# Kernel tuning notes

Hardware: AMD Instinct MI355X
Metric: run time of the kernel (lower is better)

The kernel has to match this reference:

```python
import jax, jax.numpy as jnp
import numpy as np
import math

B, N, C = 4, 4096, 1024
H, K_LM = 16, 256
HEAD_DIM = C // H


def setup_inputs() -> dict:
    key = jax.random.key(0)
    k1, k2, k3, k4, k5 = jax.random.split(key, 5)
    x = jax.random.normal(k1, (B, N, C), dtype=jnp.float32)
    Wqkv = jax.random.normal(k2, (3 * C, C), dtype=jnp.float32) * 0.02
    E = jax.random.normal(k3, (H, K_LM, N), dtype=jnp.float32) * 0.02
    Wproj = jax.random.normal(k4, (C, C), dtype=jnp.float32) * 0.02
    bproj = jax.random.normal(k5, (C,), dtype=jnp.float32) * 0.02
    return {"x": x, "Wqkv": Wqkv, "E": E, "Wproj": Wproj, "bproj": bproj}


def reference(x, Wqkv, E, Wproj, bproj):
    Bsz, n, c = x.shape
    h, d = H, c // H
    # qkv projection (no bias): [B,N,3C] -> (3,B,H,N,d)
    qkv = (x @ Wqkv.T).reshape(Bsz, n, 3, h, d).transpose(2, 0, 3, 1, 4)
    q, k, v = qkv[0], qkv[1], qkv[2]
    # Linformer landmark projection: E[h,k,n] @ K/V[b,h,n,d] -> [b,h,k,d]
    k_lm = jnp.einsum('hkn,bhnd->bhkd', E, k)
    v_lm = jnp.einsum('hkn,bhnd->bhkd', E, v)
    # scaled dot + softmax over landmarks: [b,h,n,k]
    dot = jnp.einsum('bhnd,bhkd->bhnk', q, k_lm) / math.sqrt(d)
    attn = jax.nn.softmax(dot, axis=-1)
    # weighted sum; faithful to original: reshape (B,H,N,d) -> (B,N,C) WITHOUT head transpose
    out = jnp.einsum('bhnk,bhkd->bhnd', attn, v_lm).reshape(Bsz, n, c)
    # output projection (dropouts are identity at eval / p=0)
    return out @ Wproj.T + bproj
```

## Files before the change

### kernel.cpp

```cpp
#include <hip/hip_runtime.h>


typedef unsigned short ushort_t;
typedef float f32x4 __attribute__((ext_vector_type(4)));
typedef __bf16 bf16x8 __attribute__((ext_vector_type(8)));
typedef unsigned short ushort8 __attribute__((ext_vector_type(8)));
typedef unsigned short ushort4_t __attribute__((ext_vector_type(4)));

__device__ inline ushort_t f2bf(float f) {
  unsigned int u = __float_as_uint(f);
  u += 0x7fff + ((u >> 16) & 1);
  return (ushort_t)(u >> 16);
}

__device__ inline void gload_lds16(const ushort_t* g, ushort_t* l) {
  __builtin_amdgcn_global_load_lds(
      (const __attribute__((address_space(1))) void*)g,
      (__attribute__((address_space(3))) void*)l, 16, 0, 0);
}

__global__ __launch_bounds__(256) void cvt_all(
    const float* __restrict__ x,  ushort_t* __restrict__ xo,
    const float* __restrict__ w1, ushort_t* __restrict__ w1o,
    const float* __restrict__ e,  ushort_t* __restrict__ eo,
    const float* __restrict__ w2, ushort_t* __restrict__ w2o) {
  int i = blockIdx.x * blockDim.x + threadIdx.x;
  const float* in; ushort_t* out; int idx;
  if (i < 4194304)               { in = x;  out = xo;  idx = i; }
  else if (i < 4980736)          { in = w1; out = w1o; idx = i - 4194304; }
  else if (i < 9175040)          { in = e;  out = eo;  idx = i - 4980736; }
  else                           { in = w2; out = w2o; idx = i - 9175040; }
  float4 v = ((const float4*)in)[idx];
  ushort4_t o;
  o.x = f2bf(v.x); o.y = f2bf(v.y); o.z = f2bf(v.z); o.w = f2bf(v.w);
  ((ushort4_t*)out)[idx] = o;
}


#define BARX __builtin_amdgcn_s_barrier()
#define WVM(n) do { asm volatile("s_waitcnt vmcnt(" #n ")" ::: "memory"); \
                    __builtin_amdgcn_sched_barrier(0); } while (0)
#define WLG  do { asm volatile("s_waitcnt lgkmcnt(0)" ::: "memory"); \
                  __builtin_amdgcn_sched_barrier(0); } while (0)

#define STG_A(h, slot, tt) do { \
    gload_lds16(sA[h][0] + (tt) * 64, (ushort_t*)(smem + (slot) * 32768 + (h) * 16384 + (w * 2 + 0) * 1024)); \
    gload_lds16(sA[h][1] + (tt) * 64, (ushort_t*)(smem + (slot) * 32768 + (h) * 16384 + (w * 2 + 1) * 1024)); \
  } while (0)
#define STG_B(h, slot, tt) do { \
    gload_lds16(sB[h][0] + (tt) * 64, (ushort_t*)(smem + 65536 + (slot) * 32768 + (h) * 16384 + (w * 2 + 0) * 1024)); \
    gload_lds16(sB[h][1] + (tt) * 64, (ushort_t*)(smem + 65536 + (slot) * 32768 + (h) * 16384 + (w * 2 + 1) * 1024)); \
  } while (0)

#define RD_A(mh) do { \
    const char* ba_ = smem + sl * 32768 + ((mh) * 128 + wm * 64 + l15) * 128; \
    _Pragma("unroll") for (int i_ = 0; i_ < 4; i_++) { \
      aF[i_][0] = *(const bf16x8*)(ba_ + i_ * 2048 + cs0); \
      aF[i_][1] = *(const bf16x8*)(ba_ + i_ * 2048 + cs1); } \
  } while (0)
#define RD_B(nh) do { \
    const char* bb_ = smem + 65536 + sl * 32768 + ((nh) * 128 + wn * 32 + l15) * 128; \
    _Pragma("unroll") for (int j_ = 0; j_ < 2; j_++) { \
      bF[j_][0] = *(const bf16x8*)(bb_ + j_ * 2048 + cs0); \
      bF[j_][1] = *(const bf16x8*)(bb_ + j_ * 2048 + cs1); } \
  } while (0)

#define MQ(mh, nh) do { \
    _Pragma("unroll") for (int i_ = 0; i_ < 4; i_++) \
    _Pragma("unroll") for (int j_ = 0; j_ < 2; j_++) { \
      acc[(mh) * 4 + i_][(nh) * 2 + j_] = __builtin_amdgcn_mfma_f32_16x16x32_bf16( \
          aF[i_][0], bF[j_][0], acc[(mh) * 4 + i_][(nh) * 2 + j_], 0, 0, 0); \
      acc[(mh) * 4 + i_][(nh) * 2 + j_] = __builtin_amdgcn_mfma_f32_16x16x32_bf16( \
          aF[i_][1], bF[j_][1], acc[(mh) * 4 + i_][(nh) * 2 + j_], 0, 0, 0); } \
  } while (0)

__device__ __attribute__((always_inline)) inline void pipe256(
    const ushort_t* __restrict__ Ag, const ushort_t* __restrict__ Bg,
    long long m0, long long n0, char* smem, f32x4 acc[8][4]) {
  const int tid = threadIdx.x, lane = tid & 63, w = tid >> 6;
  const int l15 = lane & 15, quad = lane >> 4;
  const int wm = w >> 2, wn = w & 3;
  const int sw = l15 & 7;
  const int K = 1024;
  const int cs0 = ((0 * 4 + quad) ^ sw) << 4;
  const int cs1 = ((1 * 4 + quad) ^ sw) << 4;
  const int lr8 = lane >> 3;
  const int sdat = ((lane & 7) ^ lr8) * 8;
  const ushort_t* sA[2][2];
  const ushort_t* sB[2][2];
#pragma unroll
  for (int h = 0; h < 2; h++)
#pragma unroll
    for (int q = 0; q < 2; q++) {
      sA[h][q] = Ag + (m0 + h * 128 + (w * 2 + q) * 8 + lr8) * K + sdat;
      sB[h][q] = Bg + (n0 + h * 128 + (w * 2 + q) * 8 + lr8) * K + sdat;
    }

  const f32x4 zz = {0.f, 0.f, 0.f, 0.f};
#pragma unroll
  for (int i = 0; i < 8; i++)
#pragma unroll
    for (int j = 0; j < 4; j++) acc[i][j] = zz;

  bf16x8 aF[4][2];
  bf16x8 bF[2][2];

  STG_A(0, 0, 0); STG_B(0, 0, 0); STG_A(1, 0, 0); STG_B(1, 0, 0);
  WVM(4);
  BARX;

#pragma unroll 2
  for (int t = 0; t < 16; ++t) {
    const int sl = t & 1, sn = sl ^ 1;
    const bool pf = (t < 15);
    RD_A(0); RD_B(0);
    if (pf) STG_A(0, sn, t + 1);
    BARX; WLG;
    __builtin_amdgcn_s_setprio(1); MQ(0, 0); __builtin_amdgcn_s_setprio(0);
    if (pf) { WVM(4); } else { WVM(2); }
    BARX;
    RD_A(1);
    if (pf) STG_B(0, sn, t + 1);
    BARX; WLG;
    __builtin_amdgcn_s_setprio(1); MQ(1, 0); __builtin_amdgcn_s_setprio(0);
    if (pf) { WVM(4); } else { WVM(0); }
    BARX;
    RD_B(1);
    if (pf) STG_A(1, sn, t + 1);
    BARX; WLG;
    __builtin_amdgcn_s_setprio(1); MQ(1, 1); __builtin_amdgcn_s_setprio(0);
    BARX;
    RD_A(0);
    if (pf) STG_B(1, sn, t + 1);
    BARX; WLG;
    __builtin_amdgcn_s_setprio(1); MQ(0, 1); __builtin_amdgcn_s_setprio(0);
    if (pf) WVM(4);
    BARX;
  }
}

__global__ __launch_bounds__(512) void gemm_qkv(
    const ushort_t* __restrict__ A, const ushort_t* __restrict__ W,
    ushort_t* __restrict__ q, ushort_t* __restrict__ kT, ushort_t* __restrict__ vT) {
  __shared__ __align__(16) char smem[131072];
  const int lin = blockIdx.x;
  const int xcd = lin & 7, rr_ = lin >> 3;
  const int mt = xcd * 8 + (rr_ & 7);
  const int nt = rr_ >> 3;
  const long long m0 = (long long)mt * 256;
  const long long n0 = (long long)nt * 256;

  f32x4 acc[8][4];
  pipe256(A, W, m0, n0, smem, acc);

  const int tid = threadIdx.x, lane = tid & 63, w = tid >> 6;
  const int l15 = lane & 15, quad = lane >> 4;
  const int wm = w >> 2, wn = w & 3;
  const int b     = (int)(m0 >> 12);
  const int nrow0 = (int)(m0 & 4095);
  const int s     = (int)(n0 >> 10);
  const int ncol0 = (int)(n0 & 1023);
  const int h0    = ncol0 >> 6;

  if (s == 0) {
#pragma unroll
    for (int mh = 0; mh < 2; mh++)
#pragma unroll
      for (int i = 0; i < 4; i++)
#pragma unroll
        for (int nh = 0; nh < 2; nh++)
#pragma unroll
          for (int j = 0; j < 2; j++) {
            int cx = ncol0 + nh * 128 + wn * 32 + j * 16;
            int h  = cx >> 6;
            int dd = (cx & 63) + l15;
            long long z = (long long)b * 16 + h;
            int nb = nrow0 + mh * 128 + wm * 64 + i * 16 + quad * 4;
#pragma unroll
            for (int r = 0; r < 4; r++)
              q[z * 262144 + (long long)(nb + r) * 64 + dd] = f2bf(acc[mh * 4 + i][nh * 2 + j][r]);
          }
  } else {
    ushort_t (*T)[136] = (ushort_t(*)[136])smem;
    ushort_t* KV = (s == 1) ? kT : vT;
#pragma unroll
    for (int p = 0; p < 2; p++) {
      __syncthreads();
#pragma unroll
      for (int i = 0; i < 4; i++)
#pragma unroll
        for (int nh = 0; nh < 2; nh++)
#pragma unroll
          for (int j = 0; j < 2; j++) {
            int c = nh * 128 + wn * 32 + j * 16 + l15;
            int t = wm * 64 + i * 16 + quad * 4;
            ushort4_t o = {f2bf(acc[p * 4 + i][nh * 2 + j][0]), f2bf(acc[p * 4 + i][nh * 2 + j][1]),
                           f2bf(acc[p * 4 + i][nh * 2 + j][2]), f2bf(acc[p * 4 + i][nh * 2 + j][3])};
            *(ushort4_t*)(&T[c][t]) = o;
          }
      __syncthreads();
#pragma unroll
      for (int it = 0; it < 8; it++) {
        int ch = it * 512 + tid;
        int cl = ch >> 4, tc = (ch & 15) * 8;
        ushort8 v = *(const ushort8*)(&T[cl][tc]);
        int h = h0 + (cl >> 6), dd = cl & 63;
        long long z = (long long)b * 16 + h;
        *(ushort8*)(KV + z * 262144 + (long long)dd * 4096 + (nrow0 + p * 128 + tc)) = v;
      }
    }
  }
}

__global__ __launch_bounds__(256) void lm_gemm(
    const ushort_t* __restrict__ E, const ushort_t* __restrict__ kT,
    const ushort_t* __restrict__ vT, float* __restrict__ pK, float* __restrict__ pV) {
  __shared__ __align__(16) ushort_t smem[12288];
  const int tid = threadIdx.x, lane = tid & 63, w = tid >> 6;
  const int l15 = lane & 15, quad = lane >> 4;
  const int kt = blockIdx.x;
  const int s  = blockIdx.y;
  const int z  = blockIdx.z;
  const int h  = z & 15;
  const int lr = lane >> 2, lc = (lane & 3) * 8;

  const ushort_t* gE = E  + ((long long)h * 256 + kt * 64 + 16 * w + lr) * 4096 + s * 1024 + lc;
  const ushort_t* gK = kT + ((long long)z * 64 + 16 * w + lr) * 4096 + s * 1024 + lc;
  const ushort_t* gV = vT + ((long long)z * 64 + 16 * w + lr) * 4096 + s * 1024 + lc;
  ushort_t* lE = smem + 512 * w;
  ushort_t* lK = smem + 4096 + 512 * w;
  ushort_t* lV = smem + 8192 + 512 * w;

  const f32x4 zz = {0.f, 0.f, 0.f, 0.f};
  f32x4 aK[4], aV[4];
#pragma unroll
  for (int j = 0; j < 4; j++) { aK[j] = zz; aV[j] = zz; }

  for (int n = 0; n < 1024; n += 64) {
    __syncthreads();
#pragma unroll
    for (int p = 0; p < 2; p++) {
      gload_lds16(gE + n + 32 * p, lE + p * 2048);
      gload_lds16(gK + n + 32 * p, lK + p * 2048);
      gload_lds16(gV + n + 32 * p, lV + p * 2048);
    }
    __syncthreads();
#pragma unroll
    for (int p = 0; p < 2; p++) {
      bf16x8 ef = *(const bf16x8*)(smem + p * 2048 + (w * 16 + l15) * 32 + quad * 8);
#pragma unroll
      for (int j = 0; j < 4; j++) {
        bf16x8 kf = *(const bf16x8*)(smem + 4096 + p * 2048 + (j * 16 + l15) * 32 + quad * 8);
        aK[j] = __builtin_amdgcn_mfma_f32_16x16x32_bf16(ef, kf, aK[j], 0, 0, 0);
        bf16x8 vf = *(const bf16x8*)(smem + 8192 + p * 2048 + (j * 16 + l15) * 32 + quad * 8);
        aV[j] = __builtin_amdgcn_mfma_f32_16x16x32_bf16(ef, vf, aV[j], 0, 0, 0);
      }
    }
  }

  float* oK = pK + ((long long)(z * 4 + s) * 256 + kt * 64) * 64;
  float* oV = pV + ((long long)(z * 4 + s) * 256 + kt * 64) * 64;
#pragma unroll
  for (int j = 0; j < 4; j++)
#pragma unroll
    for (int r = 0; r < 4; r++) {
      int row = w * 16 + quad * 4 + r, col = j * 16 + l15;
      oK[row * 64 + col] = aK[j][r];
      oV[row * 64 + col] = aV[j][r];
    }
}

__global__ __launch_bounds__(256) void lm_reduce(
    const float* __restrict__ pK, const float* __restrict__ pV,
    ushort_t* __restrict__ klm, ushort_t* __restrict__ vlmT) {
  __shared__ float Tv[64][68];
  const int tid = threadIdx.x;
  const int kt = blockIdx.x;
  const int z  = blockIdx.y;
  const long long base = (long long)z * 4 * 16384 + kt * 64 * 64;
  const int row = tid >> 2, c0 = (tid & 3) * 16;

  float sk[16];
#pragma unroll
  for (int g = 0; g < 4; g++) {
    f32x4 a = {0.f, 0.f, 0.f, 0.f};
#pragma unroll
    for (int s = 0; s < 4; s++)
      a += *(const f32x4*)(pK + base + (long long)s * 16384 + row * 64 + c0 + g * 4);
    sk[g * 4 + 0] = a[0]; sk[g * 4 + 1] = a[1]; sk[g * 4 + 2] = a[2]; sk[g * 4 + 3] = a[3];
  }
  {
    ushort_t* dst = klm + ((long long)z * 256 + kt * 64 + row) * 64 + c0;
    ushort8 o0, o1;
#pragma unroll
    for (int i = 0; i < 8; i++) { o0[i] = f2bf(sk[i]); o1[i] = f2bf(sk[8 + i]); }
    *(ushort8*)(dst) = o0;
    *(ushort8*)(dst + 8) = o1;
  }

#pragma unroll
  for (int g = 0; g < 4; g++) {
    f32x4 a = {0.f, 0.f, 0.f, 0.f};
#pragma unroll
    for (int s = 0; s < 4; s++)
      a += *(const f32x4*)(pV + base + (long long)s * 16384 + row * 64 + c0 + g * 4);
    *(f32x4*)(&Tv[row][c0 + g * 4]) = a;
  }
  __syncthreads();
  {
    ushort8 o0, o1;
#pragma unroll
    for (int i = 0; i < 8; i++) {
      o0[i] = f2bf(Tv[c0 + i][row]);
      o1[i] = f2bf(Tv[c0 + 8 + i][row]);
    }
    ushort_t* dst = vlmT + ((long long)z * 64 + row) * 256 + kt * 64 + c0;
    *(ushort8*)(dst) = o0;
    *(ushort8*)(dst + 8) = o1;
  }
}

__global__ __launch_bounds__(256) void attn_fused(
    const ushort_t* __restrict__ Q, const ushort_t* __restrict__ Klm,
    const ushort_t* __restrict__ VlmT, ushort_t* __restrict__ O) {
  __shared__ __align__(16) ushort_t smem[16896];
  ushort_t (*As)[40]  = (ushort_t(*)[40])smem;
  ushort_t (*Bs)[40]  = (ushort_t(*)[40])(smem + 2560);
  ushort_t (*P)[264]  = (ushort_t(*)[264])smem;
  const int tid = threadIdx.x, lane = tid & 63, w = tid >> 6;
  const int l15 = lane & 15, quad = lane >> 4;
  const int z = blockIdx.z;
  const long long m0 = (long long)blockIdx.x * 64;
  const ushort_t* Qb = Q + (long long)z * 262144;
  const ushort_t* Kb = Klm + (long long)z * 16384;
  const ushort_t* Vb = VlmT + (long long)z * 16384;

  const f32x4 zz = {0.f, 0.f, 0.f, 0.f};
  f32x4 acc[16];
#pragma unroll
  for (int j = 0; j < 16; j++) acc[j] = zz;

  const int sr = tid >> 2, sc = (tid & 3) * 8;

  for (int kt = 0; kt < 2; kt++) {
    const int k0 = kt * 32;
    ushort8 av = *(const ushort8*)(Qb + (m0 + sr) * 64 + k0 + sc);
    ushort8 bv[4];
#pragma unroll
    for (int r = 0; r < 4; r++) {
      int c = r * 256 + tid;
      bv[r] = *(const ushort8*)(Kb + (c >> 2) * 64 + k0 + (c & 3) * 8);
    }
    __syncthreads();
    *(ushort8*)(&As[sr][sc]) = av;
#pragma unroll
    for (int r = 0; r < 4; r++) {
      int c = r * 256 + tid;
      *(ushort8*)(&Bs[c >> 2][(c & 3) * 8]) = bv[r];
    }
    __syncthreads();
    bf16x8 af = *(const bf16x8*)(&As[w * 16 + l15][quad * 8]);
#pragma unroll
    for (int j = 0; j < 16; j++) {
      bf16x8 bfj = *(const bf16x8*)(&Bs[j * 16 + l15][quad * 8]);
      acc[j] = __builtin_amdgcn_mfma_f32_16x16x32_bf16(af, bfj, acc[j], 0, 0, 0);
    }
  }

  __syncthreads();
#pragma unroll
  for (int r = 0; r < 4; r++) {
    float x[16];
    float vmax = -1e30f;
#pragma unroll
    for (int j = 0; j < 16; j++) { x[j] = acc[j][r] * 0.125f; vmax = fmaxf(vmax, x[j]); }
#pragma unroll
    for (int m = 1; m < 16; m <<= 1) vmax = fmaxf(vmax, __shfl_xor(vmax, m, 64));
    float s = 0.f;
#pragma unroll
    for (int j = 0; j < 16; j++) { x[j] = __expf(x[j] - vmax); s += x[j]; }
#pragma unroll
    for (int m = 1; m < 16; m <<= 1) s += __shfl_xor(s, m, 64);
    float inv = 1.0f / s;
    int row = w * 16 + quad * 4 + r;
#pragma unroll
    for (int j = 0; j < 16; j++)
      P[row][j * 16 + l15] = f2bf(x[j] * inv);
  }
  __syncthreads();

  f32x4 o_acc[4];
#pragma unroll
  for (int j = 0; j < 4; j++) o_acc[j] = zz;
#pragma unroll
  for (int kc = 0; kc < 8; kc++) {
    bf16x8 pf = *(const bf16x8*)(&P[w * 16 + l15][kc * 32 + quad * 8]);
#pragma unroll
    for (int j = 0; j < 4; j++) {
      bf16x8 vf = *(const bf16x8*)(Vb + (j * 16 + l15) * 256 + kc * 32 + quad * 8);
      o_acc[j] = __builtin_amdgcn_mfma_f32_16x16x32_bf16(pf, vf, o_acc[j], 0, 0, 0);
    }
  }

#pragma unroll
  for (int j = 0; j < 4; j++)
#pragma unroll
    for (int r = 0; r < 4; r++) {
      int row = w * 16 + quad * 4 + r;
      int col = j * 16 + l15;
      O[(long long)z * 262144 + (m0 + row) * 64 + col] = f2bf(o_acc[j][r]);
    }
}

__global__ __launch_bounds__(512) void gemm_nt_256(
    const ushort_t* __restrict__ A, const ushort_t* __restrict__ B,
    float* __restrict__ C, const float* __restrict__ bias) {
  __shared__ __align__(16) char smem[131072];
  const int lin = blockIdx.x;
  const int xcd = lin & 7, rr_ = lin >> 3;
  const int mt = xcd * 8 + (rr_ & 7);
  const int nt = rr_ >> 3;
  const long long m0 = (long long)mt * 256;
  const long long n0 = (long long)nt * 256;

  f32x4 acc[8][4];
  pipe256(A, B, m0, n0, smem, acc);

  const int tid = threadIdx.x, lane = tid & 63, w = tid >> 6;
  const int l15 = lane & 15, quad = lane >> 4;
  const int wm = w >> 2, wn = w & 3;

#pragma unroll
  for (int mh = 0; mh < 2; mh++)
#pragma unroll
    for (int i = 0; i < 4; i++)
#pragma unroll
      for (int nh = 0; nh < 2; nh++)
#pragma unroll
        for (int j = 0; j < 2; j++) {
          long long row = m0 + mh * 128 + wm * 64 + i * 16 + quad * 4;
          long long col = n0 + nh * 128 + wn * 32 + j * 16 + l15;
          float bv = bias[col];
#pragma unroll
          for (int r = 0; r < 4; r++)
            C[(row + r) * 1024 + col] = acc[mh * 4 + i][nh * 2 + j][r] + bv;
        }
}

extern "C" void kernel_launch(void* const* d_in, const int* in_sizes, int n_in,
                              void* d_out, int out_size, void* d_ws, size_t ws_size,
                              hipStream_t stream) {
  const float* x     = (const float*)d_in[0];
  const float* Wqkv  = (const float*)d_in[1];
  const float* E     = (const float*)d_in[2];
  const float* Wproj = (const float*)d_in[3];
  const float* bproj = (const float*)d_in[4];
  float* out = (float*)d_out;

  char* ws = (char*)d_ws;
  ushort_t* x_bf     = (ushort_t*)(ws + 0);
  float*    pK       = (float*)   (ws + 0);
  float*    pV       = (float*)   (ws + 16777216);
  ushort_t* wqkv_bf  = (ushort_t*)(ws + 33554432);
  ushort_t* e_bf     = (ushort_t*)(ws + 39845888);
  ushort_t* wproj_bf = (ushort_t*)(ws + 73400320);
  ushort_t* q_bf     = (ushort_t*)(ws + 75497472);
  ushort_t* kT       = (ushort_t*)(ws + 109051904);
  ushort_t* vT       = (ushort_t*)(ws + 142606336);
  ushort_t* klm      = (ushort_t*)(ws + 176160768);
  ushort_t* vlmT     = (ushort_t*)(ws + 178257920);

  cvt_all<<<36864, 256, 0, stream>>>(x, x_bf, Wqkv, wqkv_bf, E, e_bf, Wproj, wproj_bf);

  gemm_qkv<<<768, 512, 0, stream>>>(x_bf, wqkv_bf, q_bf, kT, vT);

  lm_gemm<<<dim3(4, 4, 64), 256, 0, stream>>>(e_bf, kT, vT, pK, pV);

  lm_reduce<<<dim3(4, 64), 256, 0, stream>>>(pK, pV, klm, vlmT);

  attn_fused<<<dim3(64, 1, 64), 256, 0, stream>>>(q_bf, klm, vlmT, x_bf);

  gemm_nt_256<<<256, 512, 0, stream>>>(x_bf, wproj_bf, out, bproj);
}
```

Measured before the change: 451.8 us.

## Fuse landmark GEMM with reduction and reorder GEMM pipeline sub-tile schedule

Replaces the split-K landmark projection (lm_gemm plus lm_reduce through fp32 partial buffers) with a single lm_fused kernel. Each block now loops over the full N, double-buffers its LDS with async global-to-LDS loads, uses swizzled LDS addressing, and remaps blocks so each XCD handles a contiguous set of heads. This removes the fp32 partial round-trip and one launch, at the cost of fewer blocks (256) each running a longer serial loop. Separately, the main 256x256 GEMM pipeline keeps two B fragments in registers so sub-tiles run in the order (0,0),(0,1),(1,0),(1,1), cutting LDS re-reads. The last iteration is peeled to drop the per-iteration prefetch predicate.

Result: slower. 519.6 us (+15.0%).

```diff
diff --git a/kernel.cpp b/kernel.cpp
--- a/kernel.cpp
+++ b/kernel.cpp
@@ -58,20 +58,20 @@
       aF[i_][0] = *(const bf16x8*)(ba_ + i_ * 2048 + cs0); \
       aF[i_][1] = *(const bf16x8*)(ba_ + i_ * 2048 + cs1); } \
   } while (0)
-#define RD_B(nh) do { \
+#define RD_B(nh, BF) do { \
     const char* bb_ = smem + 65536 + sl * 32768 + ((nh) * 128 + wn * 32 + l15) * 128; \
     _Pragma("unroll") for (int j_ = 0; j_ < 2; j_++) { \
-      bF[j_][0] = *(const bf16x8*)(bb_ + j_ * 2048 + cs0); \
-      bF[j_][1] = *(const bf16x8*)(bb_ + j_ * 2048 + cs1); } \
+      BF[j_][0] = *(const bf16x8*)(bb_ + j_ * 2048 + cs0); \
+      BF[j_][1] = *(const bf16x8*)(bb_ + j_ * 2048 + cs1); } \
   } while (0)
 
-#define MQ(mh, nh) do { \
+#define MQ(mh, nh, BF) do { \
     _Pragma("unroll") for (int i_ = 0; i_ < 4; i_++) \
     _Pragma("unroll") for (int j_ = 0; j_ < 2; j_++) { \
       acc[(mh) * 4 + i_][(nh) * 2 + j_] = __builtin_amdgcn_mfma_f32_16x16x32_bf16( \
-          aF[i_][0], bF[j_][0], acc[(mh) * 4 + i_][(nh) * 2 + j_], 0, 0, 0); \
+          aF[i_][0], BF[j_][0], acc[(mh) * 4 + i_][(nh) * 2 + j_], 0, 0, 0); \
       acc[(mh) * 4 + i_][(nh) * 2 + j_] = __builtin_amdgcn_mfma_f32_16x16x32_bf16( \
-          aF[i_][1], bF[j_][1], acc[(mh) * 4 + i_][(nh) * 2 + j_], 0, 0, 0); } \
+          aF[i_][1], BF[j_][1], acc[(mh) * 4 + i_][(nh) * 2 + j_], 0, 0, 0); } \
   } while (0)
 
 __device__ __attribute__((always_inline)) inline void pipe256(
@@ -103,39 +103,54 @@
     for (int j = 0; j < 4; j++) acc[i][j] = zz;
 
   bf16x8 aF[4][2];
-  bf16x8 bF[2][2];
-
-  STG_A(0, 0, 0); STG_B(0, 0, 0); STG_A(1, 0, 0); STG_B(1, 0, 0);
+  bf16x8 bF0[2][2], bF1[2][2];
+
+  STG_A(0, 0, 0); STG_B(0, 0, 0); STG_B(1, 0, 0); STG_A(1, 0, 0);
   WVM(4);
   BARX;
 
 #pragma unroll 2
-  for (int t = 0; t < 16; ++t) {
+  for (int t = 0; t < 15; ++t) {
     const int sl = t & 1, sn = sl ^ 1;
-    const bool pf = (t < 15);
-    RD_A(0); RD_B(0);
-    if (pf) STG_A(0, sn, t + 1);
-    BARX; WLG;
-    __builtin_amdgcn_s_setprio(1); MQ(0, 0); __builtin_amdgcn_s_setprio(0);
-    if (pf) { WVM(4); } else { WVM(2); }
+    RD_A(0); RD_B(0, bF0);
+    STG_A(0, sn, t + 1);
+    BARX; WLG;
+    __builtin_amdgcn_s_setprio(1); MQ(0, 0, bF0); __builtin_amdgcn_s_setprio(0);
+    WVM(4);
+    BARX;
+    RD_B(1, bF1);
+    STG_B(0, sn, t + 1);
+    BARX; WLG;
+    __builtin_amdgcn_s_setprio(1); MQ(0, 1, bF1); __builtin_amdgcn_s_setprio(0);
+    WVM(4);
     BARX;
     RD_A(1);
-    if (pf) STG_B(0, sn, t + 1);
-    BARX; WLG;
-    __builtin_amdgcn_s_setprio(1); MQ(1, 0); __builtin_amdgcn_s_setprio(0);
-    if (pf) { WVM(4); } else { WVM(0); }
-    BARX;
-    RD_B(1);
-    if (pf) STG_A(1, sn, t + 1);
-    BARX; WLG;
-    __builtin_amdgcn_s_setprio(1); MQ(1, 1); __builtin_amdgcn_s_setprio(0);
-    BARX;
-    RD_A(0);
-    if (pf) STG_B(1, sn, t + 1);
-    BARX; WLG;
-    __builtin_amdgcn_s_setprio(1); MQ(0, 1); __builtin_amdgcn_s_setprio(0);
-    if (pf) WVM(4);
-    BARX;
+    STG_B(1, sn, t + 1);
+    BARX; WLG;
+    __builtin_amdgcn_s_setprio(1); MQ(1, 0, bF0); __builtin_amdgcn_s_setprio(0);
+    BARX;
+    STG_A(1, sn, t + 1);
+    __builtin_amdgcn_s_setprio(1); MQ(1, 1, bF1); __builtin_amdgcn_s_setprio(0);
+    WVM(4);
+    BARX;
+  }
+  {
+    const int sl = 1;
+    RD_A(0); RD_B(0, bF0);
+    BARX; WLG;
+    __builtin_amdgcn_s_setprio(1); MQ(0, 0, bF0); __builtin_amdgcn_s_setprio(0);
+    WVM(2);
+    BARX;
+    RD_B(1, bF1);
+    BARX; WLG;
+    __builtin_amdgcn_s_setprio(1); MQ(0, 1, bF1); __builtin_amdgcn_s_setprio(0);
+    WVM(0);
+    BARX;
+    RD_A(1);
+    BARX; WLG;
+    __builtin_amdgcn_s_setprio(1); MQ(1, 0, bF0); __builtin_amdgcn_s_setprio(0);
+    BARX;
+    __builtin_amdgcn_s_setprio(1); MQ(1, 1, bF1); __builtin_amdgcn_s_setprio(0);
   }
 }
 
@@ -212,102 +227,83 @@
   }
 }
 
-__global__ __launch_bounds__(256) void lm_gemm(
+#define LM_STAGE(s_, n_) do { \
+    ushort_t* b_ = (ushort_t*)(smemc + (s_) * 24576); \
+    _Pragma("unroll") for (int p_ = 0; p_ < 2; p_++) { \
+      gload_lds16(gE + (n_) + 32 * p_, b_ + 512 * w + p_ * 2048); \
+      gload_lds16(gK + (n_) + 32 * p_, b_ + 4096 + 512 * w + p_ * 2048); \
+      gload_lds16(gV + (n_) + 32 * p_, b_ + 8192 + 512 * w + p_ * 2048); \
+    } } while (0)
+
+#define LM_COMP(sl_) do { \
+    const ushort_t* base_ = (const ushort_t*)(smemc + (sl_) * 24576); \
+    _Pragma("unroll") for (int p_ = 0; p_ < 2; p_++) { \
+      bf16x8 ef = *(const bf16x8*)(base_ + p_ * 2048 + (w * 16 + l15) * 32 + ((quad ^ swz) * 8)); \
+      _Pragma("unroll") for (int j_ = 0; j_ < 4; j_++) { \
+        bf16x8 kf = *(const bf16x8*)(base_ + 4096 + p_ * 2048 + (j_ * 16 + l15) * 32 + ((quad ^ swz) * 8)); \
+        aK[j_] = __builtin_amdgcn_mfma_f32_16x16x32_bf16(ef, kf, aK[j_], 0, 0, 0); \
+        bf16x8 vf = *(const bf16x8*)(base_ + 8192 + p_ * 2048 + (j_ * 16 + l15) * 32 + ((quad ^ swz) * 8)); \
+        aV[j_] = __builtin_amdgcn_mfma_f32_16x16x32_bf16(ef, vf, aV[j_], 0, 0, 0); \
+      } } } while (0)
+
+__global__ __launch_bounds__(256) void lm_fused(
     const ushort_t* __restrict__ E, const ushort_t* __restrict__ kT,
-    const ushort_t* __restrict__ vT, float* __restrict__ pK, float* __restrict__ pV) {
-  __shared__ __align__(16) ushort_t smem[12288];
+    const ushort_t* __restrict__ vT, ushort_t* __restrict__ klm,
+    ushort_t* __restrict__ vlmT) {
+  __shared__ __align__(16) char smemc[49152];
   const int tid = threadIdx.x, lane = tid & 63, w = tid >> 6;
   const int l15 = lane & 15, quad = lane >> 4;
-  const int kt = blockIdx.x;
-  const int s  = blockIdx.y;
-  const int z  = blockIdx.z;
+  const int bid = blockIdx.x;
+  const int xcd = bid & 7, loc = bid >> 3;
+  const int z  = xcd * 8 + (loc >> 2);
+  const int kt = loc & 3;
   const int h  = z & 15;
-  const int lr = lane >> 2, lc = (lane & 3) * 8;
-
-  const ushort_t* gE = E  + ((long long)h * 256 + kt * 64 + 16 * w + lr) * 4096 + s * 1024 + lc;
-  const ushort_t* gK = kT + ((long long)z * 64 + 16 * w + lr) * 4096 + s * 1024 + lc;
-  const ushort_t* gV = vT + ((long long)z * 64 + 16 * w + lr) * 4096 + s * 1024 + lc;
-  ushort_t* lE = smem + 512 * w;
-  ushort_t* lK = smem + 4096 + 512 * w;
-  ushort_t* lV = smem + 8192 + 512 * w;
+  const int lr = lane >> 2;
+  const int lc = ((lane & 3) ^ ((lr >> 1) & 3)) * 8;
+  const int swz = (l15 >> 1) & 3;
+
+  const ushort_t* gE = E  + ((long long)h * 256 + kt * 64 + 16 * w + lr) * 4096 + lc;
+  const ushort_t* gK = kT + ((long long)z * 64 + 16 * w + lr) * 4096 + lc;
+  const ushort_t* gV = vT + ((long long)z * 64 + 16 * w + lr) * 4096 + lc;
 
   const f32x4 zz = {0.f, 0.f, 0.f, 0.f};
   f32x4 aK[4], aV[4];
 #pragma unroll
   for (int j = 0; j < 4; j++) { aK[j] = zz; aV[j] = zz; }
 
-  for (int n = 0; n < 1024; n += 64) {
-    __syncthreads();
-#pragma unroll
-    for (int p = 0; p < 2; p++) {
-      gload_lds16(gE + n + 32 * p, lE + p * 2048);
-      gload_lds16(gK + n + 32 * p, lK + p * 2048);
-      gload_lds16(gV + n + 32 * p, lV + p * 2048);
-    }
-    __syncthreads();
-#pragma unroll
-    for (int p = 0; p < 2; p++) {
-      bf16x8 ef = *(const bf16x8*)(smem + p * 2048 + (w * 16 + l15) * 32 + quad * 8);
-#pragma unroll
-      for (int j = 0; j < 4; j++) {
-        bf16x8 kf = *(const bf16x8*)(smem + 4096 + p * 2048 + (j * 16 + l15) * 32 + quad * 8);
-        aK[j] = __builtin_amdgcn_mfma_f32_16x16x32_bf16(ef, kf, aK[j], 0, 0, 0);
-        bf16x8 vf = *(const bf16x8*)(smem + 8192 + p * 2048 + (j * 16 + l15) * 32 + quad * 8);
-        aV[j] = __builtin_amdgcn_mfma_f32_16x16x32_bf16(ef, vf, aV[j], 0, 0, 0);
-      }
-    }
-  }
-
-  float* oK = pK + ((long long)(z * 4 + s) * 256 + kt * 64) * 64;
-  float* oV = pV + ((long long)(z * 4 + s) * 256 + kt * 64) * 64;
+  LM_STAGE(0, 0);
+#pragma unroll 2
+  for (int t = 0; t < 63; ++t) {
+    const int sl = t & 1;
+    LM_STAGE(sl ^ 1, (t + 1) * 64);
+    WVM(6);
+    BARX;
+    LM_COMP(sl);
+    BARX;
+  }
+  WVM(0);
+  BARX;
+  LM_COMP(1);
+
+  ushort_t* oK = klm + ((long long)z * 256 + kt * 64) * 64;
 #pragma unroll
   for (int j = 0; j < 4; j++)
 #pragma unroll
     for (int r = 0; r < 4; r++) {
       int row = w * 16 + quad * 4 + r, col = j * 16 + l15;
-      oK[row * 64 + col] = aK[j][r];
-      oV[row * 64 + col] = aV[j][r];
-    }
-}
-
-__global__ __launch_bounds__(256) void lm_reduce(
-    const float* __restrict__ pK, const float* __restrict__ pV,
-    ushort_t* __restrict__ klm, ushort_t* __restrict__ vlmT) {
-  __shared__ float Tv[64][68];
-  const int tid = threadIdx.x;
-  const int kt = blockIdx.x;
-  const int z  = blockIdx.y;
-  const long long base = (long long)z * 4 * 16384 + kt * 64 * 64;
-  const int row = tid >> 2, c0 = (tid & 3) * 16;
-
-  float sk[16];
-#pragma unroll
-  for (int g = 0; g < 4; g++) {
-    f32x4 a = {0.f, 0.f, 0.f, 0.f};
-#pragma unroll
-    for (int s = 0; s < 4; s++)
-      a += *(const f32x4*)(pK + base + (long long)s * 16384 + row * 64 + c0 + g * 4);
-    sk[g * 4 + 0] = a[0]; sk[g * 4 + 1] = a[1]; sk[g * 4 + 2] = a[2]; sk[g * 4 + 3] = a[3];
-  }
-  {
-    ushort_t* dst = klm + ((long long)z * 256 + kt * 64 + row) * 64 + c0;
-    ushort8 o0, o1;
-#pragma unroll
-    for (int i = 0; i < 8; i++) { o0[i] = f2bf(sk[i]); o1[i] = f2bf(sk[8 + i]); }
-    *(ushort8*)(dst) = o0;
-    *(ushort8*)(dst + 8) = o1;
-  }
-
-#pragma unroll
-  for (int g = 0; g < 4; g++) {
-    f32x4 a = {0.f, 0.f, 0.f, 0.f};
-#pragma unroll
-    for (int s = 0; s < 4; s++)
-      a += *(const f32x4*)(pV + base + (long long)s * 16384 + row * 64 + c0 + g * 4);
-    *(f32x4*)(&Tv[row][c0 + g * 4]) = a;
-  }
+      oK[row * 64 + col] = f2bf(aK[j][r]);
+    }
+
+  __syncthreads();
+  float (*Tv)[68] = (float(*)[68])smemc;
+#pragma unroll
+  for (int j = 0; j < 4; j++)
+#pragma unroll
+    for (int r = 0; r < 4; r++)
+      Tv[w * 16 + quad * 4 + r][j * 16 + l15] = aV[j][r];
   __syncthreads();
   {
+    const int row = tid >> 2, c0 = (tid & 3) * 16;
     ushort8 o0, o1;
 #pragma unroll
     for (int i = 0; i < 8; i++) {
@@ -459,8 +455,6 @@
 
   char* ws = (char*)d_ws;
   ushort_t* x_bf     = (ushort_t*)(ws + 0);
-  float*    pK       = (float*)   (ws + 0);
-  float*    pV       = (float*)   (ws + 16777216);
   ushort_t* wqkv_bf  = (ushort_t*)(ws + 33554432);
   ushort_t* e_bf     = (ushort_t*)(ws + 39845888);
   ushort_t* wproj_bf = (ushort_t*)(ws + 73400320);
@@ -474,9 +468,7 @@
 
   gemm_qkv<<<768, 512, 0, stream>>>(x_bf, wqkv_bf, q_bf, kT, vT);
 
-  lm_gemm<<<dim3(4, 4, 64), 256, 0, stream>>>(e_bf, kT, vT, pK, pV);
-
-  lm_reduce<<<dim3(4, 64), 256, 0, stream>>>(pK, pV, klm, vlmT);
+  lm_fused<<<256, 256, 0, stream>>>(e_bf, kT, vT, klm, vlmT);
 
   attn_fused<<<dim3(64, 1, 64), 256, 0, stream>>>(q_bf, klm, vlmT, x_bf);
 
```
